# Kernel tuning notes

Measured on AMD Instinct MI355X. Metric: run time of the kernel, lower is better.

The kernel has to match this reference:

```python
import jax, jax.numpy as jnp
import numpy as np

NUM_CLASSES = 2
THRESHOLD = 0.35
NEGPOS_RATIO = 7
VARIANCES = (0.1, 0.2)
B, P, O = 64, 16800, 64  # batch, num_priors, num_objs per image


def point_form(pr):
    # cxcywh -> xyxy
    return jnp.concatenate([pr[:, :2] - pr[:, 2:] / 2, pr[:, :2] + pr[:, 2:] / 2], axis=1)


def jaccard(a, b):
    # a: [A,4] xyxy, b: [Bx,4] xyxy -> IoU [A,Bx]
    lt = jnp.maximum(a[:, None, :2], b[None, :, :2])
    rb = jnp.minimum(a[:, None, 2:], b[None, :, 2:])
    wh = jnp.clip(rb - lt, 0.0)
    inter = wh[..., 0] * wh[..., 1]
    area_a = ((a[:, 2] - a[:, 0]) * (a[:, 3] - a[:, 1]))[:, None]
    area_b = ((b[:, 2] - b[:, 0]) * (b[:, 3] - b[:, 1]))[None, :]
    return inter / (area_a + area_b - inter)


def encode(matched, priors):
    # matched xyxy [P,4], priors cxcywh [P,4]
    g_cxcy = (matched[:, :2] + matched[:, 2:]) / 2 - priors[:, :2]
    g_cxcy = g_cxcy / (VARIANCES[0] * priors[:, 2:])
    g_wh = (matched[:, 2:] - matched[:, :2]) / priors[:, 2:]
    g_wh = jnp.log(g_wh) / VARIANCES[1]
    return jnp.concatenate([g_cxcy, g_wh], axis=1)


def encode_landm(matched, priors):
    # matched [P,10] -> [P,5,2]
    m = matched.reshape(-1, 5, 2)
    g = (m - priors[:, None, :2]) / (VARIANCES[0] * priors[:, None, 2:])
    return g.reshape(-1, 10)


def match_one(truths, labels, landms, priors):
    # truths [O,4], labels [O], landms [O,10]
    overlaps = jaccard(truths, point_form(priors))  # [O,P]
    best_prior_overlap = overlaps.max(axis=1)       # per-gt best IoU
    best_prior_idx = overlaps.argmax(axis=1)
    valid_gt = best_prior_overlap >= 0.2
    best_truth_overlap = overlaps.max(axis=0)       # per-prior best IoU
    best_truth_idx = overlaps.argmax(axis=0)
    # index_fill(2) only for valid gts (best_prior_idx_filter)
    bto = best_truth_overlap.at[best_prior_idx].set(
        jnp.where(valid_gt, 2.0, best_truth_overlap[best_prior_idx]))
    # ensure every gt keeps its best prior
    bti = best_truth_idx.at[best_prior_idx].set(jnp.arange(truths.shape[0]))
    matches = truths[bti]                  # [P,4]
    conf = labels[bti]                     # [P]
    conf = jnp.where(bto < THRESHOLD, 0.0, conf)
    loc = encode(matches, priors)
    landm = encode_landm(landms[bti], priors)
    return loc, conf, landm


def smooth_l1_sum(x, mask):
    ax = jnp.abs(x)
    v = jnp.where(ax < 1.0, 0.5 * ax * ax, ax - 0.5)
    return (v * mask).sum()


def setup_inputs() -> dict:
    key = jax.random.key(0)
    k1, k2, k3, k4, k5, k6, k7, k8 = jax.random.split(key, 8)
    loc_data = jax.random.normal(k1, (B, P, 4), jnp.float32)
    conf_data = jax.random.normal(k2, (B, P, NUM_CLASSES), jnp.float32)
    landm_data = jax.random.normal(k3, (B, P, 10), jnp.float32)
    # priors: cx,cy in (0,1), w,h in (0.02,0.22)
    cxy = jax.random.uniform(k4, (P, 2), jnp.float32)
    wh = jax.random.uniform(k5, (P, 2), jnp.float32) * 0.2 + 0.02
    priors = jnp.concatenate([cxy, wh], axis=1)
    # targets: valid corner boxes + landmarks + label in {1,-1}
    xy1 = jax.random.uniform(k6, (B, O, 2), jnp.float32) * 0.6
    bwh = jax.random.uniform(k7, (B, O, 2), jnp.float32) * 0.3 + 0.05
    boxes = jnp.concatenate([xy1, xy1 + bwh], axis=-1)
    lms = jax.random.uniform(k8, (B, O, 10), jnp.float32)
    lab = jnp.where(jax.random.uniform(jax.random.fold_in(key, 9), (B, O, 1)) < 0.3, -1.0, 1.0)
    targets = jnp.concatenate([boxes, lms, lab], axis=-1)
    return {"loc_data": loc_data, "conf_data": conf_data, "landm_data": landm_data,
            "priors": priors, "targets": targets}


def reference(loc_data, conf_data, landm_data, priors, targets):
    num = loc_data.shape[0]
    num_priors = priors.shape[0]
    truths = targets[:, :, :4]
    landms = targets[:, :, 4:14]
    labels = targets[:, :, -1]
    loc_t, conf_t, landm_t = jax.vmap(match_one, in_axes=(0, 0, 0, None))(
        truths, labels, landms, priors)  # [B,P,4], [B,P], [B,P,10]

    # landmark loss over conf_t > 0
    pos1 = conf_t > 0
    num_pos_landm = pos1.astype(jnp.int32).sum(axis=1, keepdims=True)
    N1 = jnp.maximum(num_pos_landm.sum().astype(jnp.float32), 1.0)
    loss_landm = smooth_l1_sum(landm_data - landm_t, pos1[..., None].astype(landm_data.dtype))

    # localization loss over conf_t != 0 ; conf_t[pos] = 1
    pos = conf_t != 0
    conf_t01 = jnp.where(pos, 1, 0)  # int {0,1}
    loss_l = smooth_l1_sum(loc_data - loc_t, pos[..., None].astype(loc_data.dtype))

    # hard negative mining on per-prior CE loss (global-max log_sum_exp, as in source)
    batch_conf = conf_data.reshape(-1, NUM_CLASSES)
    x_max = batch_conf.max()
    lse = jnp.log(jnp.exp(batch_conf - x_max).sum(axis=1, keepdims=True)) + x_max
    gathered = jnp.take_along_axis(batch_conf, conf_t01.reshape(-1, 1), axis=1)
    loss_c = (lse - gathered).reshape(num, -1)  # [B,P]; positives NOT zeroed (as in source)
    loss_idx = jnp.argsort(-loss_c, axis=1)
    idx_rank = jnp.argsort(loss_idx, axis=1)
    num_pos = pos.astype(jnp.int32).sum(axis=1, keepdims=True)  # [B,1]
    num_neg = jnp.minimum(NEGPOS_RATIO * num_pos, num_priors - 1)
    neg = idx_rank < num_neg  # [B,P]
    neg_pos = pos | neg

    # cross-entropy (sum) over selected pos+neg priors
    logp = jax.nn.log_softmax(conf_data, axis=-1)  # [B,P,C]
    ce = -jnp.take_along_axis(logp, conf_t01[..., None], axis=-1)[..., 0]
    loss_c_final = (ce * neg_pos.astype(ce.dtype)).sum()

    N = jnp.maximum(num_pos.sum().astype(jnp.float32), 1.0)
    return (loss_l / N, loss_c_final / N, loss_landm / N1)
```

## Files before the change

kernel.cpp:

```cpp
#include <hip/hip_runtime.h>
#include <math.h>

#define BN 64
#define PN 16800
#define ON 64
#define THRESH 0.35f
#define NEGPOS 7
#define GX 66
#define NBLK (BN * GX)
#define TG 4

__device__ __forceinline__ unsigned f2key(float f) {
  unsigned u = __float_as_uint(f);
  return (u & 0x80000000u) ? ~u : (u | 0x80000000u);
}
__device__ __forceinline__ float key2f(unsigned k) {
  unsigned u = (k & 0x80000000u) ? (k & 0x7FFFFFFFu) : ~k;
  return __uint_as_float(u);
}

struct Acc {
  unsigned xmax_key;
};

__device__ __forceinline__ float sl1(float d) {
  float a = fabsf(d);
  return (a < 1.f) ? 0.5f * a * a : a - 0.5f;
}

__global__ void k_best_truth(const float* __restrict__ priors,
                             const float* __restrict__ targets,
                             const float* __restrict__ conf,
                             float* __restrict__ bto, int* __restrict__ bti,
                             unsigned* __restrict__ bmax) {
  int b = blockIdx.y;
  int tid = threadIdx.x;
  int p = blockIdx.x * 256 + tid;
  float cmax = -INFINITY;
  if (p < PN) {
    float2 c2 = reinterpret_cast<const float2*>(conf)[(long)b * PN + p];
    cmax = fmaxf(c2.x, c2.y);
    float4 pr = reinterpret_cast<const float4*>(priors)[p];
    float px1 = pr.x - pr.z * 0.5f, py1 = pr.y - pr.w * 0.5f;
    float px2 = pr.x + pr.z * 0.5f, py2 = pr.y + pr.w * 0.5f;
    float area_b = (px2 - px1) * (py2 - py1);
    float bi = -1.f, bu = 1.f;
    int bidx = 0;
    const float* tgb = &targets[(long)b * ON * 15];
    for (int t = 0; t < ON; t++) {
      float ax1 = tgb[t * 15 + 0], ay1 = tgb[t * 15 + 1];
      float ax2 = tgb[t * 15 + 2], ay2 = tgb[t * 15 + 3];
      float lx = fmaxf(ax1, px1), ly = fmaxf(ay1, py1);
      float rx = fminf(ax2, px2), ry = fminf(ay2, py2);
      float w = fmaxf(rx - lx, 0.f), h = fmaxf(ry - ly, 0.f);
      float inter = w * h;
      float area_a = (ax2 - ax1) * (ay2 - ay1);
      float uni = area_a + area_b - inter;
      if (inter * bu > bi * uni) { bi = inter; bu = uni; bidx = t; }
    }
    bto[b * PN + p] = bi / bu;
    bti[b * PN + p] = bidx;
  }
  for (int off = 32; off; off >>= 1) cmax = fmaxf(cmax, __shfl_down(cmax, off));
  __shared__ float wm[4];
  if ((tid & 63) == 0) wm[tid >> 6] = cmax;
  __syncthreads();
  if (tid == 0)
    bmax[b * GX + blockIdx.x] = f2key(fmaxf(fmaxf(wm[0], wm[1]), fmaxf(wm[2], wm[3])));
}

__global__ void k_best_prior(const float* __restrict__ priors,
                             const float* __restrict__ targets,
                             float* __restrict__ bpo, int* __restrict__ bpi) {
  int bx = blockIdx.x;
  int b = bx >> 4;
  int t0 = (bx & 15) * TG;
  int tid = threadIdx.x;
  float ax1[TG], ay1[TG], ax2[TG], ay2[TG], area_a[TG];
#pragma unroll
  for (int i = 0; i < TG; i++) {
    const float* tg = &targets[((long)b * ON + t0 + i) * 15];
    ax1[i] = tg[0]; ay1[i] = tg[1]; ax2[i] = tg[2]; ay2[i] = tg[3];
    area_a[i] = (ax2[i] - ax1[i]) * (ay2[i] - ay1[i]);
  }
  float bi[TG], bu[TG]; int bp[TG];
#pragma unroll
  for (int i = 0; i < TG; i++) { bi[i] = -1.f; bu[i] = 1.f; bp[i] = 0x7FFFFFFF; }
  for (int p = tid; p < PN; p += 256) {
    float4 pr = reinterpret_cast<const float4*>(priors)[p];
    float px1 = pr.x - pr.z * 0.5f, py1 = pr.y - pr.w * 0.5f;
    float px2 = pr.x + pr.z * 0.5f, py2 = pr.y + pr.w * 0.5f;
    float area_b = (px2 - px1) * (py2 - py1);
#pragma unroll
    for (int i = 0; i < TG; i++) {
      float lx = fmaxf(ax1[i], px1), ly = fmaxf(ay1[i], py1);
      float rx = fminf(ax2[i], px2), ry = fminf(ay2[i], py2);
      float w = fmaxf(rx - lx, 0.f), h = fmaxf(ry - ly, 0.f);
      float inter = w * h;
      float uni = area_a[i] + area_b - inter;
      if (inter * bu[i] > bi[i] * uni) { bi[i] = inter; bu[i] = uni; bp[i] = p; }
    }
  }
#pragma unroll
  for (int off = 1; off < 64; off <<= 1) {
#pragma unroll
    for (int i = 0; i < TG; i++) {
      float oi = __shfl_xor(bi[i], off), ou = __shfl_xor(bu[i], off);
      int op = __shfl_xor(bp[i], off);
      float a = oi * bu[i], c = bi[i] * ou;
      if (a > c || (a == c && op < bp[i])) { bi[i] = oi; bu[i] = ou; bp[i] = op; }
    }
  }
  __shared__ float si[TG][4], su[TG][4];
  __shared__ int sp[TG][4];
  int w = tid >> 6;
  if ((tid & 63) == 0) {
#pragma unroll
    for (int i = 0; i < TG; i++) { si[i][w] = bi[i]; su[i][w] = bu[i]; sp[i][w] = bp[i]; }
  }
  __syncthreads();
  if (tid < TG) {
    float fi = si[tid][0], fu = su[tid][0]; int fp = sp[tid][0];
    for (int ww = 1; ww < 4; ww++) {
      float a = si[tid][ww] * fu, c = fi * su[tid][ww];
      if (a > c || (a == c && sp[tid][ww] < fp)) { fi = si[tid][ww]; fu = su[tid][ww]; fp = sp[tid][ww]; }
    }
    bpo[(long)b * ON + t0 + tid] = fi / fu;
    bpi[(long)b * ON + t0 + tid] = fp;
  }
}

__global__ void k_scatter(const unsigned* __restrict__ bmax,
                          const float* __restrict__ bpo, const int* __restrict__ bpi,
                          float* __restrict__ bto, int* __restrict__ bti, Acc* acc) {
  int tid = threadIdx.x;
  if (blockIdx.x == 16) {
    unsigned mk = 0;
    for (int i = tid; i < NBLK; i += 256) { unsigned v = bmax[i]; if (v > mk) mk = v; }
    for (int off = 1; off < 64; off <<= 1) {
      unsigned o = (unsigned)__shfl_xor((int)mk, off);
      if (o > mk) mk = o;
    }
    __shared__ unsigned wm[4];
    if ((tid & 63) == 0) wm[tid >> 6] = mk;
    __syncthreads();
    if (tid == 0) {
      unsigned m = wm[0];
      if (wm[1] > m) m = wm[1];
      if (wm[2] > m) m = wm[2];
      if (wm[3] > m) m = wm[3];
      acc->xmax_key = m;
    }
    return;
  }
  int row = blockIdx.x * 4 + (tid >> 6);
  int t = tid & 63;
  int q = bpi[row * ON + t];
  bool valid = bpo[row * ON + t] >= 0.2f;
  bool dupLater = false;
  for (int j = 0; j < 64; j++) {
    int ij = __shfl(q, j);
    if (j > t && ij == q) dupLater = true;
  }
  if (!dupLater) {
    bti[(long)row * PN + q] = t;
    if (valid) bto[(long)row * PN + q] = 2.0f;
  }
}

__global__ void k_encode(const float* __restrict__ loc_data,
                         const float* __restrict__ conf_data,
                         const float* __restrict__ landm_data,
                         const float* __restrict__ priors,
                         const float* __restrict__ targets,
                         const float* __restrict__ bto, const int* __restrict__ bti,
                         float* __restrict__ lossc, unsigned char* __restrict__ posf,
                         const Acc* __restrict__ acc,
                         float* __restrict__ part_l, float* __restrict__ part_lm,
                         int* __restrict__ np_part, int* __restrict__ np1_part) {
  int b = blockIdx.y;
  int p = blockIdx.x * 256 + threadIdx.x;
  int bid = b * GX + blockIdx.x;
  float sum_l = 0.f, sum_lm = 0.f;
  int cp = 0, cp1 = 0;
  if (p < PN) {
    int t = bti[b * PN + p];
    float ov = bto[b * PN + p];
    const float* tg = &targets[(b * ON + t) * 15];
    float label = tg[14];
    float conf = (ov < THRESH) ? 0.f : label;
    bool pos = (conf != 0.f);
    bool pos1 = (conf > 0.f);
    float4 pr = reinterpret_cast<const float4*>(priors)[p];
    if (pos) {
      float m0 = tg[0], m1 = tg[1], m2 = tg[2], m3 = tg[3];
      float g0 = ((m0 + m2) * 0.5f - pr.x) / (0.1f * pr.z);
      float g1 = ((m1 + m3) * 0.5f - pr.y) / (0.1f * pr.w);
      float g2 = logf((m2 - m0) / pr.z) / 0.2f;
      float g3 = logf((m3 - m1) / pr.w) / 0.2f;
      const float* ld = &loc_data[((long)b * PN + p) * 4];
      sum_l = sl1(ld[0] - g0) + sl1(ld[1] - g1) + sl1(ld[2] - g2) + sl1(ld[3] - g3);
      cp = 1;
    }
    if (pos1) {
      const float* lm = &landm_data[((long)b * PN + p) * 10];
      for (int i = 0; i < 5; i++) {
        float gx = (tg[4 + 2 * i] - pr.x) / (0.1f * pr.z);
        float gy = (tg[5 + 2 * i] - pr.y) / (0.1f * pr.w);
        sum_lm += sl1(lm[2 * i] - gx) + sl1(lm[2 * i + 1] - gy);
      }
      cp1 = 1;
    }
    float2 c2 = reinterpret_cast<const float2*>(conf_data)[(long)b * PN + p];
    float xmax = key2f(acc->xmax_key);
    float lse = logf(expf(c2.x - xmax) + expf(c2.y - xmax)) + xmax;
    lossc[b * PN + p] = lse - (pos ? c2.y : c2.x);
    posf[b * PN + p] = pos ? 1 : 0;
  }
  for (int off = 32; off; off >>= 1) {
    sum_l += __shfl_down(sum_l, off);
    sum_lm += __shfl_down(sum_lm, off);
    cp += __shfl_down(cp, off);
    cp1 += __shfl_down(cp1, off);
  }
  __shared__ float sl4[4], slm4[4];
  __shared__ int sp4[4], sp14[4];
  int w = threadIdx.x >> 6;
  if ((threadIdx.x & 63) == 0) { sl4[w] = sum_l; slm4[w] = sum_lm; sp4[w] = cp; sp14[w] = cp1; }
  __syncthreads();
  if (threadIdx.x == 0) {
    part_l[bid] = sl4[0] + sl4[1] + sl4[2] + sl4[3];
    part_lm[bid] = slm4[0] + slm4[1] + slm4[2] + slm4[3];
    np_part[bid] = sp4[0] + sp4[1] + sp4[2] + sp4[3];
    np1_part[bid] = sp14[0] + sp14[1] + sp14[2] + sp14[3];
  }
}

__global__ void __launch_bounds__(1024) k_select_sum(const float* __restrict__ lossc,
                                                     const unsigned char* __restrict__ posf,
                                                     const int* __restrict__ np_part,
                                                     float* __restrict__ part_c) {
  int b = blockIdx.x;
  int tid = threadIdx.x;
  __shared__ unsigned hist[256], suf[256];
  __shared__ unsigned s_chosen, s_rem;
  __shared__ int s_np;
  const float* row = &lossc[(long)b * PN];
  const unsigned char* prow = &posf[(long)b * PN];

  if (tid == 0) s_np = 0;
  __syncthreads();
  if (tid < GX) atomicAdd(&s_np, np_part[b * GX + tid]);
  __syncthreads();
  int np = s_np;
  long k = (long)NEGPOS * np;
  if (k > PN - 1) k = PN - 1;

  unsigned T = 0xFFFFFFFFu, R = 0, C = 0;
  if (k > 0) {
    unsigned prefix = 0, remaining = (unsigned)k, lastC = 0;
    for (int pass = 0; pass < 4; pass++) {
      int shift = 24 - pass * 8;
      if (tid < 256) hist[tid] = 0;
      __syncthreads();
      unsigned hmask = (pass == 0) ? 0u : (0xFFFFFFFFu << (shift + 8));
      for (int p = tid; p < PN; p += 1024) {
        unsigned key = f2key(row[p]);
        if (((key ^ prefix) & hmask) == 0)
          atomicAdd(&hist[(key >> shift) & 255], 1u);
      }
      __syncthreads();
      if (tid < 256) suf[tid] = hist[tid];
      __syncthreads();
      for (int off = 1; off < 256; off <<= 1) {
        unsigned tv = 0;
        if (tid < 256 && tid + off < 256) tv = suf[tid + off];
        __syncthreads();
        if (tid < 256) suf[tid] += tv;
        __syncthreads();
      }
      if (tid < 256) {
        unsigned nextS = (tid < 255) ? suf[tid + 1] : 0;
        if (suf[tid] >= remaining && nextS < remaining) {
          s_chosen = (unsigned)tid;
          s_rem = remaining - nextS;
        }
      }
      __syncthreads();
      prefix |= s_chosen << shift;
      remaining = s_rem;
      if (pass == 3) lastC = hist[s_chosen];
      __syncthreads();
    }
    T = prefix; R = remaining; C = lastC;
  }

  float s = 0.f;
  bool fastTies = (R > 0 && C == R);
  for (int p = tid; p < PN; p += 1024) {
    bool pos = prow[p] != 0;
    float v = row[p];
    unsigned key = f2key(v);
    bool sel = pos || (R > 0 && (key > T || (key == T && fastTies)));
    if (sel) s += v;
  }
  if (R > 0 && C != R && tid < 64) {
    unsigned running = 0;
    for (int base = 0; base < PN; base += 64) {
      int p = base + tid;
      bool tie = false, pos = false;
      float v = 0.f;
      if (p < PN) {
        v = row[p];
        tie = (f2key(v) == T);
        pos = prow[p] != 0;
      }
      unsigned long long m = __ballot(tie);
      if (tie) {
        unsigned rank = running + (unsigned)__popcll(m & ((1ull << tid) - 1));
        if (rank < R && !pos) s += v;
      }
      running += (unsigned)__popcll(m);
    }
  }
  for (int off = 32; off; off >>= 1) s += __shfl_down(s, off);
  __shared__ float ws[16];
  if ((tid & 63) == 0) ws[tid >> 6] = s;
  __syncthreads();
  if (tid == 0) {
    float tot = 0.f;
    for (int i = 0; i < 16; i++) tot += ws[i];
    part_c[b] = tot;
  }
}

__global__ void k_final(const float* __restrict__ part_l, const float* __restrict__ part_lm,
                        const float* __restrict__ part_c,
                        const int* __restrict__ np_part, const int* __restrict__ np1_part,
                        float* __restrict__ out) {
  float sl = 0.f, slm = 0.f, sc = 0.f;
  int np = 0, np1 = 0;
  for (int i = threadIdx.x; i < NBLK; i += 256) {
    sl += part_l[i]; slm += part_lm[i];
    np += np_part[i]; np1 += np1_part[i];
  }
  if (threadIdx.x < BN) sc = part_c[threadIdx.x];
  for (int off = 32; off; off >>= 1) {
    sl += __shfl_down(sl, off); slm += __shfl_down(slm, off); sc += __shfl_down(sc, off);
    np += __shfl_down(np, off); np1 += __shfl_down(np1, off);
  }
  __shared__ float a[4], bsh[4], c[4];
  __shared__ int d[4], e[4];
  int w = threadIdx.x >> 6;
  if ((threadIdx.x & 63) == 0) { a[w] = sl; bsh[w] = slm; c[w] = sc; d[w] = np; e[w] = np1; }
  __syncthreads();
  if (threadIdx.x == 0) {
    float N = fmaxf((float)(d[0] + d[1] + d[2] + d[3]), 1.f);
    float N1 = fmaxf((float)(e[0] + e[1] + e[2] + e[3]), 1.f);
    out[0] = (a[0] + a[1] + a[2] + a[3]) / N;
    out[1] = (c[0] + c[1] + c[2] + c[3]) / N;
    out[2] = (bsh[0] + bsh[1] + bsh[2] + bsh[3]) / N1;
  }
}

extern "C" void kernel_launch(void* const* d_in, const int* in_sizes, int n_in,
                              void* d_out, int out_size, void* d_ws, size_t ws_size,
                              hipStream_t stream) {
  const float* loc_data = (const float*)d_in[0];
  const float* conf_data = (const float*)d_in[1];
  const float* landm_data = (const float*)d_in[2];
  const float* priors = (const float*)d_in[3];
  const float* targets = (const float*)d_in[4];
  float* out = (float*)d_out;

  char* ws = (char*)d_ws;
  const size_t SZ = (size_t)BN * PN * 4;
  size_t off = 0;
  float* lossc = (float*)(ws + off); off += SZ;
  float* bto = (float*)(ws + off); off += SZ;
  int* bti = (int*)(ws + off); off += SZ;
  unsigned char* posf = (unsigned char*)(ws + off); off += (size_t)BN * PN;
  off = (off + 15) & ~(size_t)15;
  float* bpo = (float*)(ws + off); off += (size_t)BN * ON * 4;
  int* bpi = (int*)(ws + off); off += (size_t)BN * ON * 4;
  unsigned* bmax = (unsigned*)(ws + off); off += NBLK * 4;
  float* part_l = (float*)(ws + off); off += NBLK * 4;
  float* part_lm = (float*)(ws + off); off += NBLK * 4;
  float* part_c = (float*)(ws + off); off += BN * 4;
  int* np_part = (int*)(ws + off); off += NBLK * 4;
  int* np1_part = (int*)(ws + off); off += NBLK * 4;
  Acc* acc = (Acc*)(ws + off); off += sizeof(Acc);

  dim3 gbp(GX, BN);

  k_best_truth<<<gbp, 256, 0, stream>>>(priors, targets, conf_data, bto, bti, bmax);
  k_best_prior<<<BN * (ON / TG), 256, 0, stream>>>(priors, targets, bpo, bpi);
  k_scatter<<<17, 256, 0, stream>>>(bmax, bpo, bpi, bto, bti, acc);
  k_encode<<<gbp, 256, 0, stream>>>(loc_data, conf_data, landm_data, priors, targets,
                                    bto, bti, lossc, posf, acc,
                                    part_l, part_lm, np_part, np1_part);
  k_select_sum<<<BN, 1024, 0, stream>>>(lossc, posf, np_part, part_c);
  k_final<<<1, 256, 0, stream>>>(part_l, part_lm, part_c, np_part, np1_part, out);
}
```

Baseline: 231.2 us.

## Register-tile best-truth IoU, drop global max pass, speed up radix select scan

k_best_truth now processes four priors per thread and stages target boxes in shared memory, cutting redundant global loads. The global conf max reduction is removed, and log-sum-exp uses a per-row max instead. k_encode caches targets in shared memory and uses reciprocals with fast log/exp intrinsics. The radix-select suffix scan uses wave shuffles instead of a barrier-heavy shared loop, and equal-count ties are resolved arithmetically. Fast intrinsics and the per-row max slightly alter rounding.

```diff
diff --git a/kernel.cpp b/kernel.cpp
--- a/kernel.cpp
+++ b/kernel.cpp
@@ -8,6 +8,8 @@
 #define NEGPOS 7
 #define GX 66
 #define NBLK (BN * GX)
+#define GXB 17
+#define PT 4
 #define TG 4
 
 __device__ __forceinline__ unsigned f2key(float f) {
@@ -18,11 +20,6 @@
   unsigned u = (k & 0x80000000u) ? (k & 0x7FFFFFFFu) : ~k;
   return __uint_as_float(u);
 }
-
-struct Acc {
-  unsigned xmax_key;
-};
-
 __device__ __forceinline__ float sl1(float d) {
   float a = fabsf(d);
   return (a < 1.f) ? 0.5f * a * a : a - 0.5f;
@@ -30,43 +27,58 @@
 
 __global__ void k_best_truth(const float* __restrict__ priors,
                              const float* __restrict__ targets,
-                             const float* __restrict__ conf,
-                             float* __restrict__ bto, int* __restrict__ bti,
-                             unsigned* __restrict__ bmax) {
+                             float* __restrict__ bto, int* __restrict__ bti) {
   int b = blockIdx.y;
   int tid = threadIdx.x;
-  int p = blockIdx.x * 256 + tid;
-  float cmax = -INFINITY;
-  if (p < PN) {
-    float2 c2 = reinterpret_cast<const float2*>(conf)[(long)b * PN + p];
-    cmax = fmaxf(c2.x, c2.y);
-    float4 pr = reinterpret_cast<const float4*>(priors)[p];
-    float px1 = pr.x - pr.z * 0.5f, py1 = pr.y - pr.w * 0.5f;
-    float px2 = pr.x + pr.z * 0.5f, py2 = pr.y + pr.w * 0.5f;
-    float area_b = (px2 - px1) * (py2 - py1);
-    float bi = -1.f, bu = 1.f;
-    int bidx = 0;
-    const float* tgb = &targets[(long)b * ON * 15];
-    for (int t = 0; t < ON; t++) {
-      float ax1 = tgb[t * 15 + 0], ay1 = tgb[t * 15 + 1];
-      float ax2 = tgb[t * 15 + 2], ay2 = tgb[t * 15 + 3];
-      float lx = fmaxf(ax1, px1), ly = fmaxf(ay1, py1);
-      float rx = fminf(ax2, px2), ry = fminf(ay2, py2);
+  int base = blockIdx.x * 1024 + tid;
+
+  __shared__ float4 tbox[ON];
+  __shared__ float tarea[ON];
+  if (tid < ON) {
+    const float* tg = &targets[((long)b * ON + tid) * 15];
+    float4 bx = make_float4(tg[0], tg[1], tg[2], tg[3]);
+    tbox[tid] = bx;
+    tarea[tid] = (bx.z - bx.x) * (bx.w - bx.y);
+  }
+  __syncthreads();
+
+  float px1[PT], py1[PT], px2[PT], py2[PT], ab[PT];
+  bool val[PT];
+#pragma unroll
+  for (int i = 0; i < PT; i++) {
+    int p = base + 256 * i;
+    val[i] = p < PN;
+    float4 pr = reinterpret_cast<const float4*>(priors)[val[i] ? p : base];
+    px1[i] = pr.x - pr.z * 0.5f; py1[i] = pr.y - pr.w * 0.5f;
+    px2[i] = pr.x + pr.z * 0.5f; py2[i] = pr.y + pr.w * 0.5f;
+    ab[i] = (px2[i] - px1[i]) * (py2[i] - py1[i]);
+  }
+  float bi[PT], bu[PT]; int id[PT];
+#pragma unroll
+  for (int i = 0; i < PT; i++) { bi[i] = -1.f; bu[i] = 1.f; id[i] = 0; }
+
+#pragma unroll 4
+  for (int t = 0; t < ON; t++) {
+    float4 a = tbox[t];
+    float aa = tarea[t];
+#pragma unroll
+    for (int i = 0; i < PT; i++) {
+      float lx = fmaxf(a.x, px1[i]), ly = fmaxf(a.y, py1[i]);
+      float rx = fminf(a.z, px2[i]), ry = fminf(a.w, py2[i]);
       float w = fmaxf(rx - lx, 0.f), h = fmaxf(ry - ly, 0.f);
       float inter = w * h;
-      float area_a = (ax2 - ax1) * (ay2 - ay1);
-      float uni = area_a + area_b - inter;
-      if (inter * bu > bi * uni) { bi = inter; bu = uni; bidx = t; }
-    }
-    bto[b * PN + p] = bi / bu;
-    bti[b * PN + p] = bidx;
-  }
-  for (int off = 32; off; off >>= 1) cmax = fmaxf(cmax, __shfl_down(cmax, off));
-  __shared__ float wm[4];
-  if ((tid & 63) == 0) wm[tid >> 6] = cmax;
-  __syncthreads();
-  if (tid == 0)
-    bmax[b * GX + blockIdx.x] = f2key(fmaxf(fmaxf(wm[0], wm[1]), fmaxf(wm[2], wm[3])));
+      float uni = aa + ab[i] - inter;
+      if (inter * bu[i] > bi[i] * uni) { bi[i] = inter; bu[i] = uni; id[i] = t; }
+    }
+  }
+#pragma unroll
+  for (int i = 0; i < PT; i++) {
+    if (val[i]) {
+      int p = base + 256 * i;
+      bto[(long)b * PN + p] = bi[i] / bu[i];
+      bti[(long)b * PN + p] = id[i];
+    }
+  }
 }
 
 __global__ void k_best_prior(const float* __restrict__ priors,
@@ -112,47 +124,27 @@
     }
   }
   __shared__ float si[TG][4], su[TG][4];
-  __shared__ int sp[TG][4];
+  __shared__ int spx[TG][4];
   int w = tid >> 6;
   if ((tid & 63) == 0) {
 #pragma unroll
-    for (int i = 0; i < TG; i++) { si[i][w] = bi[i]; su[i][w] = bu[i]; sp[i][w] = bp[i]; }
+    for (int i = 0; i < TG; i++) { si[i][w] = bi[i]; su[i][w] = bu[i]; spx[i][w] = bp[i]; }
   }
   __syncthreads();
   if (tid < TG) {
-    float fi = si[tid][0], fu = su[tid][0]; int fp = sp[tid][0];
+    float fi = si[tid][0], fu = su[tid][0]; int fp = spx[tid][0];
     for (int ww = 1; ww < 4; ww++) {
       float a = si[tid][ww] * fu, c = fi * su[tid][ww];
-      if (a > c || (a == c && sp[tid][ww] < fp)) { fi = si[tid][ww]; fu = su[tid][ww]; fp = sp[tid][ww]; }
+      if (a > c || (a == c && spx[tid][ww] < fp)) { fi = si[tid][ww]; fu = su[tid][ww]; fp = spx[tid][ww]; }
     }
     bpo[(long)b * ON + t0 + tid] = fi / fu;
     bpi[(long)b * ON + t0 + tid] = fp;
   }
 }
 
-__global__ void k_scatter(const unsigned* __restrict__ bmax,
-                          const float* __restrict__ bpo, const int* __restrict__ bpi,
-                          float* __restrict__ bto, int* __restrict__ bti, Acc* acc) {
+__global__ void k_scatter(const float* __restrict__ bpo, const int* __restrict__ bpi,
+                          float* __restrict__ bto, int* __restrict__ bti) {
   int tid = threadIdx.x;
-  if (blockIdx.x == 16) {
-    unsigned mk = 0;
-    for (int i = tid; i < NBLK; i += 256) { unsigned v = bmax[i]; if (v > mk) mk = v; }
-    for (int off = 1; off < 64; off <<= 1) {
-      unsigned o = (unsigned)__shfl_xor((int)mk, off);
-      if (o > mk) mk = o;
-    }
-    __shared__ unsigned wm[4];
-    if ((tid & 63) == 0) wm[tid >> 6] = mk;
-    __syncthreads();
-    if (tid == 0) {
-      unsigned m = wm[0];
-      if (wm[1] > m) m = wm[1];
-      if (wm[2] > m) m = wm[2];
-      if (wm[3] > m) m = wm[3];
-      acc->xmax_key = m;
-    }
-    return;
-  }
   int row = blockIdx.x * 4 + (tid >> 6);
   int t = tid & 63;
   int q = bpi[row * ON + t];
@@ -175,45 +167,50 @@
                          const float* __restrict__ targets,
                          const float* __restrict__ bto, const int* __restrict__ bti,
                          float* __restrict__ lossc, unsigned char* __restrict__ posf,
-                         const Acc* __restrict__ acc,
                          float* __restrict__ part_l, float* __restrict__ part_lm,
                          int* __restrict__ np_part, int* __restrict__ np1_part) {
   int b = blockIdx.y;
   int p = blockIdx.x * 256 + threadIdx.x;
   int bid = b * GX + blockIdx.x;
+  __shared__ float4 tgs4[ON * 15 / 4];
+  float* tgs = (float*)tgs4;
+  if (threadIdx.x < ON * 15 / 4)
+    tgs4[threadIdx.x] = reinterpret_cast<const float4*>(targets + (long)b * ON * 15)[threadIdx.x];
+  __syncthreads();
   float sum_l = 0.f, sum_lm = 0.f;
   int cp = 0, cp1 = 0;
   if (p < PN) {
     int t = bti[b * PN + p];
     float ov = bto[b * PN + p];
-    const float* tg = &targets[(b * ON + t) * 15];
+    const float* tg = &tgs[t * 15];
     float label = tg[14];
-    float conf = (ov < THRESH) ? 0.f : label;
-    bool pos = (conf != 0.f);
-    bool pos1 = (conf > 0.f);
+    bool pos = ov >= THRESH;
+    bool pos1 = pos && (label > 0.f);
     float4 pr = reinterpret_cast<const float4*>(priors)[p];
     if (pos) {
+      float rz = 1.0f / pr.z, rw = 1.0f / pr.w;
       float m0 = tg[0], m1 = tg[1], m2 = tg[2], m3 = tg[3];
-      float g0 = ((m0 + m2) * 0.5f - pr.x) / (0.1f * pr.z);
-      float g1 = ((m1 + m3) * 0.5f - pr.y) / (0.1f * pr.w);
-      float g2 = logf((m2 - m0) / pr.z) / 0.2f;
-      float g3 = logf((m3 - m1) / pr.w) / 0.2f;
+      float g0 = ((m0 + m2) * 0.5f - pr.x) * rz * 10.f;
+      float g1 = ((m1 + m3) * 0.5f - pr.y) * rw * 10.f;
+      float g2 = __logf((m2 - m0) * rz) * 5.f;
+      float g3 = __logf((m3 - m1) * rw) * 5.f;
       const float* ld = &loc_data[((long)b * PN + p) * 4];
       sum_l = sl1(ld[0] - g0) + sl1(ld[1] - g1) + sl1(ld[2] - g2) + sl1(ld[3] - g3);
       cp = 1;
-    }
-    if (pos1) {
-      const float* lm = &landm_data[((long)b * PN + p) * 10];
-      for (int i = 0; i < 5; i++) {
-        float gx = (tg[4 + 2 * i] - pr.x) / (0.1f * pr.z);
-        float gy = (tg[5 + 2 * i] - pr.y) / (0.1f * pr.w);
-        sum_lm += sl1(lm[2 * i] - gx) + sl1(lm[2 * i + 1] - gy);
+      if (pos1) {
+        const float* lm = &landm_data[((long)b * PN + p) * 10];
+#pragma unroll
+        for (int i = 0; i < 5; i++) {
+          float gx = (tg[4 + 2 * i] - pr.x) * rz * 10.f;
+          float gy = (tg[5 + 2 * i] - pr.y) * rw * 10.f;
+          sum_lm += sl1(lm[2 * i] - gx) + sl1(lm[2 * i + 1] - gy);
+        }
+        cp1 = 1;
       }
-      cp1 = 1;
     }
     float2 c2 = reinterpret_cast<const float2*>(conf_data)[(long)b * PN + p];
-    float xmax = key2f(acc->xmax_key);
-    float lse = logf(expf(c2.x - xmax) + expf(c2.y - xmax)) + xmax;
+    float m = fmaxf(c2.x, c2.y);
+    float lse = m + __logf(__expf(c2.x - m) + __expf(c2.y - m));
     lossc[b * PN + p] = lse - (pos ? c2.y : c2.x);
     posf[b * PN + p] = pos ? 1 : 0;
   }
@@ -236,14 +233,15 @@
   }
 }
 
-__global__ void __launch_bounds__(1024) k_select_sum(const float* __restrict__ lossc,
-                                                     const unsigned char* __restrict__ posf,
-                                                     const int* __restrict__ np_part,
-                                                     float* __restrict__ part_c) {
+__global__ void __launch_bounds__(1024) k_select(const float* __restrict__ lossc,
+                                                 const unsigned char* __restrict__ posf,
+                                                 const int* __restrict__ np_part,
+                                                 float* __restrict__ part_c) {
   int b = blockIdx.x;
   int tid = threadIdx.x;
-  __shared__ unsigned hist[256], suf[256];
-  __shared__ unsigned s_chosen, s_rem;
+  __shared__ unsigned hist[256];
+  __shared__ unsigned wtot[4];
+  __shared__ unsigned s_d, s_rem;
   __shared__ int s_np;
   const float* row = &lossc[(long)b * PN];
   const unsigned char* prow = &posf[(long)b * PN];
@@ -252,13 +250,13 @@
   __syncthreads();
   if (tid < GX) atomicAdd(&s_np, np_part[b * GX + tid]);
   __syncthreads();
-  int np = s_np;
-  long k = (long)NEGPOS * np;
+  int k = NEGPOS * s_np;
   if (k > PN - 1) k = PN - 1;
-
-  unsigned T = 0xFFFFFFFFu, R = 0, C = 0;
-  if (k > 0) {
-    unsigned prefix = 0, remaining = (unsigned)k, lastC = 0;
+  bool haveNeg = (k > 0);
+
+  unsigned T = 0, R = 0, C = 0;
+  if (haveNeg) {
+    unsigned rem = (unsigned)k, prefix = 0;
     for (int pass = 0; pass < 4; pass++) {
       int shift = 24 - pass * 8;
       if (tid < 256) hist[tid] = 0;
@@ -270,66 +268,67 @@
           atomicAdd(&hist[(key >> shift) & 255], 1u);
       }
       __syncthreads();
-      if (tid < 256) suf[tid] = hist[tid];
+      unsigned h = (tid < 256) ? hist[tid] : 0;
+      unsigned v = h;
+      int lane = tid & 63;
+#pragma unroll
+      for (int off = 1; off < 64; off <<= 1) {
+        unsigned tv = (unsigned)__shfl_down((int)v, off);
+        if (lane + off < 64) v += tv;
+      }
+      if (tid < 256 && lane == 0) wtot[tid >> 6] = v;
       __syncthreads();
-      for (int off = 1; off < 256; off <<= 1) {
-        unsigned tv = 0;
-        if (tid < 256 && tid + off < 256) tv = suf[tid + off];
-        __syncthreads();
-        if (tid < 256) suf[tid] += tv;
-        __syncthreads();
-      }
       if (tid < 256) {
-        unsigned nextS = (tid < 255) ? suf[tid + 1] : 0;
-        if (suf[tid] >= remaining && nextS < remaining) {
-          s_chosen = (unsigned)tid;
-          s_rem = remaining - nextS;
-        }
+        unsigned add = 0;
+        for (int w2 = (tid >> 6) + 1; w2 < 4; w2++) add += wtot[w2];
+        unsigned suf = v + add;
+        if (suf >= rem && (suf - h) < rem) { s_d = (unsigned)tid; s_rem = rem - (suf - h); }
       }
       __syncthreads();
-      prefix |= s_chosen << shift;
-      remaining = s_rem;
-      if (pass == 3) lastC = hist[s_chosen];
+      prefix |= s_d << shift;
+      rem = s_rem;
+      if (pass == 3) { T = prefix; R = rem; C = hist[s_d]; }
       __syncthreads();
     }
-    T = prefix; R = remaining; C = lastC;
-  }
-
-  float s = 0.f;
-  bool fastTies = (R > 0 && C == R);
+  }
+
+  float acc = 0.f;
+  unsigned ptc = 0;
   for (int p = tid; p < PN; p += 1024) {
+    float v = row[p];
     bool pos = prow[p] != 0;
-    float v = row[p];
     unsigned key = f2key(v);
-    bool sel = pos || (R > 0 && (key > T || (key == T && fastTies)));
-    if (sel) s += v;
-  }
-  if (R > 0 && C != R && tid < 64) {
+    if (pos) acc += v;
+    else if (haveNeg && key > T) acc += v;
+    if (haveNeg && pos && key == T) ptc++;
+  }
+  if (haveNeg && C != R && tid < 64) {
     unsigned running = 0;
     for (int base = 0; base < PN; base += 64) {
       int p = base + tid;
       bool tie = false, pos = false;
       float v = 0.f;
-      if (p < PN) {
-        v = row[p];
-        tie = (f2key(v) == T);
-        pos = prow[p] != 0;
-      }
+      if (p < PN) { v = row[p]; tie = (f2key(v) == T); pos = prow[p] != 0; }
       unsigned long long m = __ballot(tie);
       if (tie) {
         unsigned rank = running + (unsigned)__popcll(m & ((1ull << tid) - 1));
-        if (rank < R && !pos) s += v;
+        if (rank < R && !pos) acc += v;
       }
       running += (unsigned)__popcll(m);
     }
   }
-  for (int off = 32; off; off >>= 1) s += __shfl_down(s, off);
-  __shared__ float ws[16];
-  if ((tid & 63) == 0) ws[tid >> 6] = s;
+  for (int off = 32; off; off >>= 1) {
+    acc += __shfl_down(acc, off);
+    ptc += __shfl_down(ptc, off);
+  }
+  __shared__ float wsum[16];
+  __shared__ unsigned wpt[16];
+  if ((tid & 63) == 0) { wsum[tid >> 6] = acc; wpt[tid >> 6] = ptc; }
   __syncthreads();
   if (tid == 0) {
-    float tot = 0.f;
-    for (int i = 0; i < 16; i++) tot += ws[i];
+    float tot = 0.f; unsigned pt = 0;
+    for (int i = 0; i < 16; i++) { tot += wsum[i]; pt += wpt[i]; }
+    if (haveNeg && C == R) tot += (float)(C - pt) * key2f(T);
     part_c[b] = tot;
   }
 }
@@ -383,22 +382,21 @@
   off = (off + 15) & ~(size_t)15;
   float* bpo = (float*)(ws + off); off += (size_t)BN * ON * 4;
   int* bpi = (int*)(ws + off); off += (size_t)BN * ON * 4;
-  unsigned* bmax = (unsigned*)(ws + off); off += NBLK * 4;
   float* part_l = (float*)(ws + off); off += NBLK * 4;
   float* part_lm = (float*)(ws + off); off += NBLK * 4;
   float* part_c = (float*)(ws + off); off += BN * 4;
   int* np_part = (int*)(ws + off); off += NBLK * 4;
   int* np1_part = (int*)(ws + off); off += NBLK * 4;
-  Acc* acc = (Acc*)(ws + off); off += sizeof(Acc);
-
+
+  dim3 gbt(GXB, BN);
   dim3 gbp(GX, BN);
 
-  k_best_truth<<<gbp, 256, 0, stream>>>(priors, targets, conf_data, bto, bti, bmax);
+  k_best_truth<<<gbt, 256, 0, stream>>>(priors, targets, bto, bti);
   k_best_prior<<<BN * (ON / TG), 256, 0, stream>>>(priors, targets, bpo, bpi);
-  k_scatter<<<17, 256, 0, stream>>>(bmax, bpo, bpi, bto, bti, acc);
+  k_scatter<<<16, 256, 0, stream>>>(bpo, bpi, bto, bti);
   k_encode<<<gbp, 256, 0, stream>>>(loc_data, conf_data, landm_data, priors, targets,
-                                    bto, bti, lossc, posf, acc,
+                                    bto, bti, lossc, posf,
                                     part_l, part_lm, np_part, np1_part);
-  k_select_sum<<<BN, 1024, 0, stream>>>(lossc, posf, np_part, part_c);
+  k_select<<<BN, 1024, 0, stream>>>(lossc, posf, np_part, part_c);
   k_final<<<1, 256, 0, stream>>>(part_l, part_lm, part_c, np_part, np1_part, out);
 }
```

Measured after the change: 222.7 us. 3.7% less time.
